# Kernel tuning notes

Measured on AMD Instinct MI355X. Metric: run time of the kernel, lower is better.

## Reference

```python
import jax
jax.config.update("jax_enable_x64", True)
import jax.numpy as jnp
import numpy as np

CKA_WEIGHT = 0.1


def _group_cka_sum(feats):
    """feats: [F, N, D] float. Returns sum of pairwise CKA over all (i,j) pairs.

    Faithful to CKASR: K = X X^T with zeroed diagonal, unbiased HSIC
    (Song et al. estimator), CKA[i,j] = HSIC(Ki,Kj)/sqrt(HSIC(Ki,Ki)HSIC(Kj,Kj)).
    All pairwise loops are batched into einsums.
    """
    F, N, D = feats.shape
    X = feats.reshape(F, N, D).astype(jnp.float64)
    K = jnp.einsum('fnd,fmd->fnm', X, X)                 # [F,N,N] Gram
    K = K * (1.0 - jnp.eye(N, dtype=K.dtype))            # fill_diagonal_(0)
    # HSIC(Ki, Kj) = 1/(N(N-3)) * ( tr(Ki Kj)
    #   + sum(Ki) sum(Kj) / ((N-1)(N-2))
    #   - 2/(N-2) * <rowsum(Ki), rowsum(Kj)> )
    trKL = jnp.einsum('iab,jab->ij', K, K)               # tr(Ki Kj), K symmetric
    s = jnp.sum(K, axis=(1, 2))                          # [F] total sums
    r = jnp.sum(K, axis=2)                               # [F,N] row sums
    rr = jnp.einsum('ia,ja->ij', r, r)                   # [F,F]
    hsic = (trKL + jnp.outer(s, s) / ((N - 1) * (N - 2))
            - 2.0 * rr / (N - 2)) / (N * (N - 3))        # [F,F]
    d = jnp.sqrt(jnp.diagonal(hsic))                     # [F]
    cka = hsic / (d[:, None] * d[None, :])
    return jnp.sum(cka)


def setup_inputs() -> dict:
    key = jax.random.key(0)
    k1, k2, k3, k4 = jax.random.split(key, 4)
    N, C = 64, 1000
    output = jax.random.normal(k1, (N, C), dtype=jnp.float32)
    target = jax.random.randint(k2, (N,), 0, C, dtype=jnp.int64)
    feats_a = jax.random.normal(k3, (3, N, 65536), dtype=jnp.float32)
    feats_b = jax.random.normal(k4, (4, N, 32768), dtype=jnp.float32)
    return {"output": output, "target": target,
            "feats_a": feats_a, "feats_b": feats_b}


def reference(output, target, feats_a, feats_b):
    N = output.shape[0]
    logp = jax.nn.log_softmax(output.astype(jnp.float32), axis=-1)
    ce = -jnp.mean(logp[jnp.arange(N), target])           # CrossEntropyLoss (mean)
    cka = _group_cka_sum(feats_a) + _group_cka_sum(feats_b)
    loss = ce + CKA_WEIGHT * cka.astype(jnp.float32)
    return (loss, output)
```

## Files before the change

kernel.cpp:

```cpp
#include <hip/hip_runtime.h>
#include <hip/hip_bf16.h>
#include <math.h>

typedef __attribute__((ext_vector_type(8))) short short8;
typedef __attribute__((ext_vector_type(4))) float f32x4;

#define NROWS 64
#define KB    128
#define ROWP  136

__global__ __launch_bounds__(256) void ce_kernel(
    const float* __restrict__ logits, const int* __restrict__ target,
    float* __restrict__ out_copy, float* __restrict__ ce_rows)
{
    const int row = blockIdx.x;
    const float* x = logits + row * 1000;
    const int t = threadIdx.x;
    __shared__ float red[256];

    float m = -INFINITY;
    for (int i = t; i < 1000; i += 256) {
        float v = x[i];
        out_copy[row * 1000 + i] = v;
        m = fmaxf(m, v);
    }
    red[t] = m; __syncthreads();
    for (int s = 128; s > 0; s >>= 1) {
        if (t < s) red[t] = fmaxf(red[t], red[t + s]);
        __syncthreads();
    }
    m = red[0];
    __syncthreads();

    float ssum = 0.f;
    for (int i = t; i < 1000; i += 256) ssum += expf(x[i] - m);
    red[t] = ssum; __syncthreads();
    for (int s = 128; s > 0; s >>= 1) {
        if (t < s) red[t] += red[t + s];
        __syncthreads();
    }
    if (t == 0) {
        double lse = (double)m + log((double)red[0]);
        int tg = target[row];
        ce_rows[row] = (float)(-((double)x[tg] - lse));
    }
}

__device__ __forceinline__ unsigned int bf16_rn(float x) {
    unsigned int u = __float_as_uint(x);
    return (u + 0x7FFFu + ((u >> 16) & 1u)) >> 16;
}

__global__ __launch_bounds__(256) void gram_kernel(
    const float* __restrict__ A, const float* __restrict__ B,
    float* __restrict__ partials, int nA, int nB)
{
    __shared__ __align__(16) char smem[2 * NROWS * ROWP * 2];
    ushort* Hi = (ushort*)smem;
    ushort* Lo = (ushort*)(smem + NROWS * ROWP * 2);
    float*  kbuf = (float*)smem;

    const int blk = blockIdx.x;
    const float* X;
    int subs, strideBlocks, c;
    if (blk < 3 * nA) {
        int f = blk / nA; c = blk % nA;
        X = A + (size_t)f * NROWS * 65536;
        subs = 65536 / KB;
        strideBlocks = nA;
    } else {
        int b2 = blk - 3 * nA;
        int f = b2 / nB; c = b2 % nB;
        X = B + (size_t)f * NROWS * 32768;
        subs = 32768 / KB;
        strideBlocks = nB;
    }
    const int D = subs * KB;

    const int t = threadIdx.x;
    const int wave = t >> 6, lane = t & 63;
    const int m = lane & 15, quad = lane >> 4;

    f32x4 acc[4][4];
#pragma unroll
    for (int i = 0; i < 4; ++i)
#pragma unroll
        for (int j = 0; j < 4; ++j) acc[i][j] = (f32x4)0.f;

    for (int s = c; s < subs; s += strideBlocks) {
        const int d0 = s * KB;
#pragma unroll
        for (int q = 0; q < 8; ++q) {
            int idx = t + q * 256;
            int row = idx >> 5;
            int k4  = idx & 31;
            float4 v = *(const float4*)(X + (size_t)row * D + d0 + (k4 << 2));
            float vv[4] = {v.x, v.y, v.z, v.w};
            unsigned int hbits[4], lbits[4];
#pragma unroll
            for (int k = 0; k < 4; ++k) {
                unsigned int hb = bf16_rn(vv[k]);
                hbits[k] = hb;
                float hf = __uint_as_float(hb << 16);
                lbits[k] = bf16_rn(vv[k] - hf);
            }
            uint2 hp2, lp2;
            hp2.x = hbits[0] | (hbits[1] << 16);
            hp2.y = hbits[2] | (hbits[3] << 16);
            lp2.x = lbits[0] | (lbits[1] << 16);
            lp2.y = lbits[2] | (lbits[3] << 16);
            int base = row * ROWP + (k4 << 2);
            *(uint2*)(Hi + base) = hp2;
            *(uint2*)(Lo + base) = lp2;
        }
        __syncthreads();
        const int koff = (wave << 5) + (quad << 3);
        const ushort* hp = Hi + m * ROWP + koff;
        const ushort* lp = Lo + m * ROWP + koff;
        short8 hf[4], lf[4];
#pragma unroll
        for (int t4 = 0; t4 < 4; ++t4) {
            hf[t4] = *(const short8*)(hp + t4 * 16 * ROWP);
            lf[t4] = *(const short8*)(lp + t4 * 16 * ROWP);
        }
#pragma unroll
        for (int tm = 0; tm < 4; ++tm)
#pragma unroll
            for (int tn = 0; tn < 4; ++tn) {
                acc[tm][tn] = __builtin_amdgcn_mfma_f32_16x16x32_bf16(
                    hf[tm], hf[tn], acc[tm][tn], 0, 0, 0);
                acc[tm][tn] = __builtin_amdgcn_mfma_f32_16x16x32_bf16(
                    hf[tm], lf[tn], acc[tm][tn], 0, 0, 0);
                acc[tm][tn] = __builtin_amdgcn_mfma_f32_16x16x32_bf16(
                    lf[tm], hf[tn], acc[tm][tn], 0, 0, 0);
            }
        __syncthreads();
    }

    if (wave == 0) {
#pragma unroll
        for (int tm = 0; tm < 4; ++tm)
#pragma unroll
            for (int tn = 0; tn < 4; ++tn)
#pragma unroll
                for (int r = 0; r < 4; ++r)
                    kbuf[(tm * 16 + quad * 4 + r) * 64 + tn * 16 + m] = acc[tm][tn][r];
    }
    __syncthreads();
    if (wave != 0) {
#pragma unroll
        for (int tm = 0; tm < 4; ++tm)
#pragma unroll
            for (int tn = 0; tn < 4; ++tn)
#pragma unroll
                for (int r = 0; r < 4; ++r)
                    atomicAdd(&kbuf[(tm * 16 + quad * 4 + r) * 64 + tn * 16 + m],
                              acc[tm][tn][r]);
    }
    __syncthreads();

    float4* outp = (float4*)(partials + (size_t)blk * 4096);
    const float4* kb4 = (const float4*)kbuf;
    for (int e = t; e < 1024; e += 256) outp[e] = kb4[e];
}

__global__ __launch_bounds__(256) void reduce_kernel(
    const float* __restrict__ partials, float* __restrict__ K, int nA, int nB)
{
    int gid = blockIdx.x * 256 + threadIdx.x;
    if (gid >= 7 * 4096) return;
    int f = gid >> 12, e = gid & 4095;
    int base, cnt;
    if (f < 3) { base = f * nA; cnt = nA; }
    else       { base = 3 * nA + (f - 3) * nB; cnt = nB; }
    double s0 = 0.0, s1 = 0.0, s2 = 0.0, s3 = 0.0;
    int j = 0;
    for (; j + 4 <= cnt; j += 4) {
        s0 += (double)partials[(size_t)(base + j + 0) * 4096 + e];
        s1 += (double)partials[(size_t)(base + j + 1) * 4096 + e];
        s2 += (double)partials[(size_t)(base + j + 2) * 4096 + e];
        s3 += (double)partials[(size_t)(base + j + 3) * 4096 + e];
    }
    for (; j < cnt; ++j) s0 += (double)partials[(size_t)(base + j) * 4096 + e];
    double sum = (s0 + s1) + (s2 + s3);
    int rr = e >> 6, cc = e & 63;
    K[gid] = (rr == cc) ? 0.f : (float)sum;
}

__global__ __launch_bounds__(256) void hsic_kernel(
    const float* __restrict__ K, double* __restrict__ hsic_out)
{
    const int p = blockIdx.x;
    int i, j;
    if (p < 9) { i = p / 3; j = p % 3; }
    else       { int q = p - 9; i = 3 + q / 4; j = 3 + q % 4; }
    const float* Ki = K + i * 4096;
    const float* Kj = K + j * 4096;
    const int t = threadIdx.x;

    __shared__ double red[256];
    __shared__ double ri[64], rj[64];

    double local = 0.0;
    for (int e = t; e < 4096; e += 256)
        local += (double)Ki[e] * (double)Kj[e];
    red[t] = local; __syncthreads();
    for (int s = 128; s > 0; s >>= 1) {
        if (t < s) red[t] += red[t + s];
        __syncthreads();
    }

    if (t < 64) {
        double s = 0.0;
        for (int mcol = 0; mcol < 64; ++mcol) s += (double)Ki[t * 64 + mcol];
        ri[t] = s;
    } else if (t < 128) {
        int n = t - 64;
        double s = 0.0;
        for (int mcol = 0; mcol < 64; ++mcol) s += (double)Kj[n * 64 + mcol];
        rj[n] = s;
    }
    __syncthreads();

    if (t == 0) {
        double tr = red[0];
        double rr = 0.0, si = 0.0, sj = 0.0;
        for (int n = 0; n < 64; ++n) {
            rr += ri[n] * rj[n];
            si += ri[n];
            sj += rj[n];
        }
        const double N = 64.0;
        const double c1 = (N - 1.0) * (N - 2.0);
        const double c2 = N - 2.0;
        const double c3 = N * (N - 3.0);
        hsic_out[p] = (tr + si * sj / c1 - 2.0 * rr / c2) / c3;
    }
}

__global__ __launch_bounds__(64) void final_kernel(
    const double* __restrict__ hsic, const float* __restrict__ ce_rows,
    float* __restrict__ out_loss)
{
    if (threadIdx.x != 0) return;
    double ce = 0.0;
    for (int n = 0; n < 64; ++n) ce += (double)ce_rows[n];
    ce /= 64.0;

    double cka_total = 0.0;
    for (int i = 0; i < 3; ++i)
        for (int j = 0; j < 3; ++j)
            cka_total += hsic[i * 3 + j] / sqrt(hsic[i * 3 + i] * hsic[j * 3 + j]);
    for (int i = 0; i < 4; ++i)
        for (int j = 0; j < 4; ++j)
            cka_total += hsic[9 + i * 4 + j] / sqrt(hsic[9 + i * 4 + i] * hsic[9 + j * 4 + j]);

    out_loss[0] = (float)(ce + 0.1 * cka_total);
}

extern "C" void kernel_launch(void* const* d_in, const int* in_sizes, int n_in,
                              void* d_out, int out_size, void* d_ws, size_t ws_size,
                              hipStream_t stream)
{
    const float* output  = (const float*)d_in[0];
    const int*   target  = (const int*)d_in[1];
    const float* feats_a = (const float*)d_in[2];
    const float* feats_b = (const float*)d_in[3];
    float* out = (float*)d_out;

    char* ws = (char*)d_ws;
    float*  K        = (float*)ws;
    float*  ce_rows  = (float*)(ws + 114688);
    double* hsic     = (double*)(ws + 114944);
    float*  partials = (float*)(ws + 131072);

    int nA = 128, nB = 64;
    for (;;) {
        size_t need = 131072 + (size_t)(3 * nA + 4 * nB) * 4096u * 4u;
        if (need <= ws_size || (nA == 1 && nB == 1)) break;
        nA = (nA > 1) ? (nA >> 1) : 1;
        nB = (nB > 1) ? (nB >> 1) : 1;
    }
    const int nblocks = 3 * nA + 4 * nB;

    hipLaunchKernelGGL(ce_kernel, dim3(64), dim3(256), 0, stream,
                       output, target, out + 1, ce_rows);
    hipLaunchKernelGGL(gram_kernel, dim3(nblocks), dim3(256), 0, stream,
                       feats_a, feats_b, partials, nA, nB);
    hipLaunchKernelGGL(reduce_kernel, dim3(112), dim3(256), 0, stream,
                       partials, K, nA, nB);
    hipLaunchKernelGGL(hsic_kernel, dim3(25), dim3(256), 0, stream,
                       K, hsic);
    hipLaunchKernelGGL(final_kernel, dim3(1), dim3(64), 0, stream,
                       hsic, ce_rows, out);
}
```

Measured before the change: 191.0 us.

## Load Gram fragments directly into registers, drop LDS staging, double block count

The Gram kernel now reads each lane's MFMA operand rows straight from global memory and splits them into bf16 hi/lo in registers. This removes the shared-memory staging and the two barriers per k-step. The partial-block count doubles to raise parallelism, and the reduce kernel splits the per-element sum across four thread groups with a shared-memory combine. The trade-offs are less coalesced global loads and more partial-sum traffic to write and reduce.

```diff
diff --git a/kernel.cpp b/kernel.cpp
--- a/kernel.cpp
+++ b/kernel.cpp
@@ -6,8 +6,6 @@
 typedef __attribute__((ext_vector_type(4))) float f32x4;
 
 #define NROWS 64
-#define KB    128
-#define ROWP  136
 
 __global__ __launch_bounds__(256) void ce_kernel(
     const float* __restrict__ logits, const int* __restrict__ target,
@@ -55,10 +53,7 @@
     const float* __restrict__ A, const float* __restrict__ B,
     float* __restrict__ partials, int nA, int nB)
 {
-    __shared__ __align__(16) char smem[2 * NROWS * ROWP * 2];
-    ushort* Hi = (ushort*)smem;
-    ushort* Lo = (ushort*)(smem + NROWS * ROWP * 2);
-    float*  kbuf = (float*)smem;
+    __shared__ float kbuf[4096];
 
     const int blk = blockIdx.x;
     const float* X;
@@ -66,16 +61,16 @@
     if (blk < 3 * nA) {
         int f = blk / nA; c = blk % nA;
         X = A + (size_t)f * NROWS * 65536;
-        subs = 65536 / KB;
+        subs = 65536 / 128;
         strideBlocks = nA;
     } else {
         int b2 = blk - 3 * nA;
         int f = b2 / nB; c = b2 % nB;
         X = B + (size_t)f * NROWS * 32768;
-        subs = 32768 / KB;
+        subs = 32768 / 128;
         strideBlocks = nB;
     }
-    const int D = subs * KB;
+    const int D = subs * 128;
 
     const int t = threadIdx.x;
     const int wave = t >> 6, lane = t & 63;
@@ -88,40 +83,26 @@
         for (int j = 0; j < 4; ++j) acc[i][j] = (f32x4)0.f;
 
     for (int s = c; s < subs; s += strideBlocks) {
-        const int d0 = s * KB;
-#pragma unroll
-        for (int q = 0; q < 8; ++q) {
-            int idx = t + q * 256;
-            int row = idx >> 5;
-            int k4  = idx & 31;
-            float4 v = *(const float4*)(X + (size_t)row * D + d0 + (k4 << 2));
-            float vv[4] = {v.x, v.y, v.z, v.w};
-            unsigned int hbits[4], lbits[4];
-#pragma unroll
-            for (int k = 0; k < 4; ++k) {
-                unsigned int hb = bf16_rn(vv[k]);
-                hbits[k] = hb;
-                float hf = __uint_as_float(hb << 16);
-                lbits[k] = bf16_rn(vv[k] - hf);
+        const int k0 = s * 128 + (wave << 5) + (quad << 3);
+        float4 fa[4], fb[4];
+#pragma unroll
+        for (int tm = 0; tm < 4; ++tm) {
+            const float* p = X + (size_t)(tm * 16 + m) * D + k0;
+            fa[tm] = *(const float4*)p;
+            fb[tm] = *(const float4*)(p + 4);
+        }
+        short8 hf[4], lf[4];
+#pragma unroll
+        for (int tm = 0; tm < 4; ++tm) {
+            float vv[8] = {fa[tm].x, fa[tm].y, fa[tm].z, fa[tm].w,
+                           fb[tm].x, fb[tm].y, fb[tm].z, fb[tm].w};
+#pragma unroll
+            for (int j = 0; j < 8; ++j) {
+                unsigned int hb = bf16_rn(vv[j]);
+                hf[tm][j] = (short)hb;
+                float hfv = __uint_as_float(hb << 16);
+                lf[tm][j] = (short)bf16_rn(vv[j] - hfv);
             }
-            uint2 hp2, lp2;
-            hp2.x = hbits[0] | (hbits[1] << 16);
-            hp2.y = hbits[2] | (hbits[3] << 16);
-            lp2.x = lbits[0] | (lbits[1] << 16);
-            lp2.y = lbits[2] | (lbits[3] << 16);
-            int base = row * ROWP + (k4 << 2);
-            *(uint2*)(Hi + base) = hp2;
-            *(uint2*)(Lo + base) = lp2;
-        }
-        __syncthreads();
-        const int koff = (wave << 5) + (quad << 3);
-        const ushort* hp = Hi + m * ROWP + koff;
-        const ushort* lp = Lo + m * ROWP + koff;
-        short8 hf[4], lf[4];
-#pragma unroll
-        for (int t4 = 0; t4 < 4; ++t4) {
-            hf[t4] = *(const short8*)(hp + t4 * 16 * ROWP);
-            lf[t4] = *(const short8*)(lp + t4 * 16 * ROWP);
         }
 #pragma unroll
         for (int tm = 0; tm < 4; ++tm)
@@ -134,9 +115,9 @@
                 acc[tm][tn] = __builtin_amdgcn_mfma_f32_16x16x32_bf16(
                     lf[tm], hf[tn], acc[tm][tn], 0, 0, 0);
             }
-        __syncthreads();
-    }
-
+    }
+
+    __syncthreads();
     if (wave == 0) {
 #pragma unroll
         for (int tm = 0; tm < 4; ++tm)
@@ -167,24 +148,32 @@
 __global__ __launch_bounds__(256) void reduce_kernel(
     const float* __restrict__ partials, float* __restrict__ K, int nA, int nB)
 {
-    int gid = blockIdx.x * 256 + threadIdx.x;
-    if (gid >= 7 * 4096) return;
-    int f = gid >> 12, e = gid & 4095;
+    __shared__ double red[256];
+    const int f = blockIdx.x >> 6;
+    const int e = ((blockIdx.x & 63) << 6) + (threadIdx.x & 63);
+    const int jg = threadIdx.x >> 6;
     int base, cnt;
     if (f < 3) { base = f * nA; cnt = nA; }
     else       { base = 3 * nA + (f - 3) * nB; cnt = nB; }
+
     double s0 = 0.0, s1 = 0.0, s2 = 0.0, s3 = 0.0;
-    int j = 0;
-    for (; j + 4 <= cnt; j += 4) {
-        s0 += (double)partials[(size_t)(base + j + 0) * 4096 + e];
-        s1 += (double)partials[(size_t)(base + j + 1) * 4096 + e];
-        s2 += (double)partials[(size_t)(base + j + 2) * 4096 + e];
-        s3 += (double)partials[(size_t)(base + j + 3) * 4096 + e];
-    }
-    for (; j < cnt; ++j) s0 += (double)partials[(size_t)(base + j) * 4096 + e];
-    double sum = (s0 + s1) + (s2 + s3);
-    int rr = e >> 6, cc = e & 63;
-    K[gid] = (rr == cc) ? 0.f : (float)sum;
+    int j = jg;
+    for (; j + 12 < cnt; j += 16) {
+        s0 += (double)partials[(size_t)(base + j)      * 4096 + e];
+        s1 += (double)partials[(size_t)(base + j + 4)  * 4096 + e];
+        s2 += (double)partials[(size_t)(base + j + 8)  * 4096 + e];
+        s3 += (double)partials[(size_t)(base + j + 12) * 4096 + e];
+    }
+    for (; j < cnt; j += 4)
+        s0 += (double)partials[(size_t)(base + j) * 4096 + e];
+    red[threadIdx.x] = (s0 + s1) + (s2 + s3);
+    __syncthreads();
+    if (jg == 0) {
+        double tot = red[threadIdx.x] + red[threadIdx.x + 64] +
+                     red[threadIdx.x + 128] + red[threadIdx.x + 192];
+        int rr = e >> 6, cc = e & 63;
+        K[f * 4096 + e] = (rr == cc) ? 0.f : (float)tot;
+    }
 }
 
 __global__ __launch_bounds__(256) void hsic_kernel(
@@ -274,7 +263,7 @@
     double* hsic     = (double*)(ws + 114944);
     float*  partials = (float*)(ws + 131072);
 
-    int nA = 128, nB = 64;
+    int nA = 256, nB = 128;
     for (;;) {
         size_t need = 131072 + (size_t)(3 * nA + 4 * nB) * 4096u * 4u;
         if (need <= ws_size || (nA == 1 && nB == 1)) break;
@@ -287,7 +276,7 @@
                        output, target, out + 1, ce_rows);
     hipLaunchKernelGGL(gram_kernel, dim3(nblocks), dim3(256), 0, stream,
                        feats_a, feats_b, partials, nA, nB);
-    hipLaunchKernelGGL(reduce_kernel, dim3(112), dim3(256), 0, stream,
+    hipLaunchKernelGGL(reduce_kernel, dim3(7 * 64), dim3(256), 0, stream,
                        partials, K, nA, nB);
     hipLaunchKernelGGL(hsic_kernel, dim3(25), dim3(256), 0, stream,
                        K, hsic);
```

Measured after the change: 203.8 us. +6.7%, slower.
